# Kernel optimization log

Measured on AMD Instinct MI355X. Metric: run time of the kernel, lower is better.

Reference implementation:

```python
import jax, jax.numpy as jnp
import numpy as np

B, N, K = 16, 4096, 128

def setup_inputs() -> dict:
    key = jax.random.key(0)
    k1, k2, k3, k4, k5 = jax.random.split(key, 5)
    positions = jax.random.normal(k1, (B, N, 3), dtype=jnp.float32) * 5.0
    neighbors = jax.random.randint(k2, (B, N, K), 0, N, dtype=jnp.int32)
    neighbor_mask = (jax.random.uniform(k3, (B, N, K)) < 0.9).astype(jnp.float32)
    cell = jax.random.normal(k4, (B, 3, 3), dtype=jnp.float32) + 10.0 * jnp.eye(3, dtype=jnp.float32)
    cell_offsets = jax.random.randint(k5, (B, N, K, 3), -1, 2).astype(jnp.float32)
    return {
        "positions": positions,
        "neighbors": neighbors,
        "neighbor_mask": neighbor_mask,
        "cell": cell,
        "cell_offsets": cell_offsets,
    }

def reference(positions, neighbors, neighbor_mask, cell, cell_offsets):
    # Gather neighbor positions: [B,N,K,3]
    pos_j = jax.vmap(lambda p, n: p[n])(positions, neighbors)
    # Relative vectors r_j - r_i
    dist_vec = pos_j - positions[:, :, None, :]
    # Periodic boundary correction: offsets @ cell, [B,N,K,3]
    dist_vec = dist_vec + jnp.einsum("bnkd,bde->bnke", cell_offsets, cell)
    sq = jnp.sum(dist_vec * dist_vec, axis=-1)  # [B,N,K]
    mask = neighbor_mask > 0
    # Masked distances (safe sqrt: avoid sqrt(0) grad issues on masked entries)
    distances = jnp.where(mask, jnp.sqrt(jnp.where(mask, sq, 1.0)), 0.0)
    return distances
```

## Files before the change

kernel.cpp:

```cpp
#include <hip/hip_runtime.h>
#include <math.h>

constexpr int B = 16;
constexpr int N = 4096;
constexpr int K = 128;

constexpr int ROWS_PER_BLOCK = 128;
constexpr int THREADS = 1024;
constexpr int CHUNKS  = 4;


struct Chunk {
    int4   jj;
    float4 mm, o0, o1, o2;
};

__device__ __forceinline__ void load_chunk(Chunk& c,
                                           const int*   __restrict__ nbr,
                                           const float* __restrict__ mask,
                                           const float* __restrict__ offs,
                                           size_t e0) {
    c.jj = *(const int4*)  (nbr  + e0);
    c.mm = *(const float4*)(mask + e0);
    c.o0 = *(const float4*)(offs + e0 * 3);
    c.o1 = *(const float4*)(offs + e0 * 3 + 4);
    c.o2 = *(const float4*)(offs + e0 * 3 + 8);
}

__global__ __launch_bounds__(THREADS, 8)
void pairwise_dist_pipe(const float* __restrict__ pos,
                        const int*   __restrict__ nbr,
                        const float* __restrict__ mask,
                        const float* __restrict__ cell,
                        const float* __restrict__ offs,
                        float*       __restrict__ out) {
    __shared__ float4 spos[N];

    const int tid   = threadIdx.x;
    const int b     = blockIdx.x >> 5;
    const int rblk  = blockIdx.x & 31;
    const int nbase = rblk * ROWS_PER_BLOCK;

    {
        const float4* __restrict__ pb4 =
            (const float4*)(pos + (size_t)b * N * 3);
        const float4 r0 = pb4[tid * 3 + 0];
        const float4 r1 = pb4[tid * 3 + 1];
        const float4 r2 = pb4[tid * 3 + 2];
        const int a0 = tid * 4;
        spos[a0 + 0] = make_float4(r0.x, r0.y, r0.z, 0.f);
        spos[a0 + 1] = make_float4(r0.w, r1.x, r1.y, 0.f);
        spos[a0 + 2] = make_float4(r1.z, r1.w, r2.x, 0.f);
        spos[a0 + 3] = make_float4(r2.y, r2.z, r2.w, 0.f);
    }

    const float* __restrict__ cb = cell + b * 9;
    const float c00 = cb[0], c01 = cb[1], c02 = cb[2];
    const float c10 = cb[3], c11 = cb[4], c12 = cb[5];
    const float c20 = cb[6], c21 = cb[7], c22 = cb[8];

    __syncthreads();

    const size_t blockElemBase = ((size_t)b * N + nbase) * K;

    Chunk cur;
    load_chunk(cur, nbr, mask, offs, blockElemBase + (size_t)tid * 4);

#pragma unroll
    for (int c = 0; c < CHUNKS; ++c) {
        Chunk nxt;
        if (c + 1 < CHUNKS) {
            const size_t eN = blockElemBase + (size_t)(c + 1) * 4096 +
                              (size_t)tid * 4;
            load_chunk(nxt, nbr, mask, offs, eN);
        }

        const int    eLocal = c * 4096 + tid * 4;
        const size_t e0     = blockElemBase + eLocal;
        const int    n      = nbase + (eLocal >> 7);
        const float4 pi     = spos[n];

        const float ox[4] = {cur.o0.x, cur.o0.w, cur.o1.z, cur.o2.y};
        const float oy[4] = {cur.o0.y, cur.o1.x, cur.o1.w, cur.o2.z};
        const float oz[4] = {cur.o0.z, cur.o1.y, cur.o2.x, cur.o2.w};
        const int   j [4] = {cur.jj.x, cur.jj.y, cur.jj.z, cur.jj.w};
        const float m [4] = {cur.mm.x, cur.mm.y, cur.mm.z, cur.mm.w};

        float res[4];
#pragma unroll
        for (int i = 0; i < 4; ++i) {
            const float4 pj = spos[j[i]];
            const float dx = (pj.x - pi.x) + ox[i] * c00 + oy[i] * c10 + oz[i] * c20;
            const float dy = (pj.y - pi.y) + ox[i] * c01 + oy[i] * c11 + oz[i] * c21;
            const float dz = (pj.z - pi.z) + ox[i] * c02 + oy[i] * c12 + oz[i] * c22;
            const float sq = dx * dx + dy * dy + dz * dz;
            res[i] = (m[i] > 0.0f) ? sqrtf(sq) : 0.0f;
        }

        *(float4*)(out + e0) = make_float4(res[0], res[1], res[2], res[3]);

        cur = nxt;
    }
}

extern "C" void kernel_launch(void* const* d_in, const int* in_sizes, int n_in,
                              void* d_out, int out_size, void* d_ws, size_t ws_size,
                              hipStream_t stream) {
    const float* positions     = (const float*)d_in[0];
    const int*   neighbors     = (const int*)  d_in[1];
    const float* neighbor_mask = (const float*)d_in[2];
    const float* cell          = (const float*)d_in[3];
    const float* cell_offsets  = (const float*)d_in[4];
    float*       out           = (float*)d_out;

    const int blocks = B * (N / ROWS_PER_BLOCK);

    pairwise_dist_pipe<<<blocks, THREADS, 0, stream>>>(
        positions, neighbors, neighbor_mask, cell, cell_offsets, out);
}
```

Before: 215.5 us.

## Deepen load pipeline to a 4-chunk window with nontemporal loads and stores

Each block now covers 256 rows in 8 chunks and keeps four chunks of neighbor, mask and offset loads in flight, instead of prefetching one chunk ahead. Streaming loads and the output store use nontemporal builtins so they do not pollute cache. The shared-memory position staging is amortized over twice as many rows, which halves the number of blocks. The costs are more registers per thread (occupancy hint lowered from 8 to 4) and only 256 blocks left to fill the GPU.

```diff
diff --git a/kernel.cpp b/kernel.cpp
--- a/kernel.cpp
+++ b/kernel.cpp
@@ -5,14 +5,18 @@
 constexpr int N = 4096;
 constexpr int K = 128;
 
-constexpr int ROWS_PER_BLOCK = 128;
+constexpr int ROWS_PER_BLOCK = 256;
 constexpr int THREADS = 1024;
-constexpr int CHUNKS  = 4;
+constexpr int CHUNKS  = 8;
+constexpr int WINDOW  = 4;
+
+typedef float fx4 __attribute__((ext_vector_type(4)));
+typedef int   ix4 __attribute__((ext_vector_type(4)));
 
 
 struct Chunk {
-    int4   jj;
-    float4 mm, o0, o1, o2;
+    ix4 jj;
+    fx4 mm, o0, o1, o2;
 };
 
 __device__ __forceinline__ void load_chunk(Chunk& c,
@@ -20,38 +24,37 @@
                                            const float* __restrict__ mask,
                                            const float* __restrict__ offs,
                                            size_t e0) {
-    c.jj = *(const int4*)  (nbr  + e0);
-    c.mm = *(const float4*)(mask + e0);
-    c.o0 = *(const float4*)(offs + e0 * 3);
-    c.o1 = *(const float4*)(offs + e0 * 3 + 4);
-    c.o2 = *(const float4*)(offs + e0 * 3 + 8);
+    c.jj = __builtin_nontemporal_load((const ix4*)(nbr  + e0));
+    c.mm = __builtin_nontemporal_load((const fx4*)(mask + e0));
+    c.o0 = __builtin_nontemporal_load((const fx4*)(offs + e0 * 3));
+    c.o1 = __builtin_nontemporal_load((const fx4*)(offs + e0 * 3 + 4));
+    c.o2 = __builtin_nontemporal_load((const fx4*)(offs + e0 * 3 + 8));
 }
 
-__global__ __launch_bounds__(THREADS, 8)
-void pairwise_dist_pipe(const float* __restrict__ pos,
-                        const int*   __restrict__ nbr,
-                        const float* __restrict__ mask,
-                        const float* __restrict__ cell,
-                        const float* __restrict__ offs,
-                        float*       __restrict__ out) {
-    __shared__ float4 spos[N];
+__global__ __launch_bounds__(THREADS, 4)
+void pairwise_dist_mlp(const float* __restrict__ pos,
+                       const int*   __restrict__ nbr,
+                       const float* __restrict__ mask,
+                       const float* __restrict__ cell,
+                       const float* __restrict__ offs,
+                       float*       __restrict__ out) {
+    __shared__ fx4 spos[N];
 
     const int tid   = threadIdx.x;
-    const int b     = blockIdx.x >> 5;
-    const int rblk  = blockIdx.x & 31;
+    const int b     = blockIdx.x >> 4;
+    const int rblk  = blockIdx.x & 15;
     const int nbase = rblk * ROWS_PER_BLOCK;
 
     {
-        const float4* __restrict__ pb4 =
-            (const float4*)(pos + (size_t)b * N * 3);
-        const float4 r0 = pb4[tid * 3 + 0];
-        const float4 r1 = pb4[tid * 3 + 1];
-        const float4 r2 = pb4[tid * 3 + 2];
+        const fx4* __restrict__ pb4 = (const fx4*)(pos + (size_t)b * N * 3);
+        const fx4 r0 = pb4[tid * 3 + 0];
+        const fx4 r1 = pb4[tid * 3 + 1];
+        const fx4 r2 = pb4[tid * 3 + 2];
         const int a0 = tid * 4;
-        spos[a0 + 0] = make_float4(r0.x, r0.y, r0.z, 0.f);
-        spos[a0 + 1] = make_float4(r0.w, r1.x, r1.y, 0.f);
-        spos[a0 + 2] = make_float4(r1.z, r1.w, r2.x, 0.f);
-        spos[a0 + 3] = make_float4(r2.y, r2.z, r2.w, 0.f);
+        spos[a0 + 0] = (fx4){r0.x, r0.y, r0.z, 0.f};
+        spos[a0 + 1] = (fx4){r0.w, r1.x, r1.y, 0.f};
+        spos[a0 + 2] = (fx4){r1.z, r1.w, r2.x, 0.f};
+        spos[a0 + 3] = (fx4){r2.y, r2.z, r2.w, 0.f};
     }
 
     const float* __restrict__ cb = cell + b * 9;
@@ -63,22 +66,25 @@
 
     const size_t blockElemBase = ((size_t)b * N + nbase) * K;
 
-    Chunk cur;
-    load_chunk(cur, nbr, mask, offs, blockElemBase + (size_t)tid * 4);
+    Chunk win[WINDOW];
+#pragma unroll
+    for (int c = 0; c < WINDOW; ++c)
+        load_chunk(win[c], nbr, mask, offs,
+                   blockElemBase + (size_t)c * 4096 + (size_t)tid * 4);
 
 #pragma unroll
     for (int c = 0; c < CHUNKS; ++c) {
-        Chunk nxt;
-        if (c + 1 < CHUNKS) {
-            const size_t eN = blockElemBase + (size_t)(c + 1) * 4096 +
-                              (size_t)tid * 4;
-            load_chunk(nxt, nbr, mask, offs, eN);
-        }
+        const Chunk cur = win[c % WINDOW];
 
         const int    eLocal = c * 4096 + tid * 4;
         const size_t e0     = blockElemBase + eLocal;
         const int    n      = nbase + (eLocal >> 7);
-        const float4 pi     = spos[n];
+        const fx4    pi     = spos[n];
+
+        if (c + WINDOW < CHUNKS)
+            load_chunk(win[c % WINDOW], nbr, mask, offs,
+                       blockElemBase + (size_t)(c + WINDOW) * 4096 +
+                       (size_t)tid * 4);
 
         const float ox[4] = {cur.o0.x, cur.o0.w, cur.o1.z, cur.o2.y};
         const float oy[4] = {cur.o0.y, cur.o1.x, cur.o1.w, cur.o2.z};
@@ -89,7 +95,7 @@
         float res[4];
 #pragma unroll
         for (int i = 0; i < 4; ++i) {
-            const float4 pj = spos[j[i]];
+            const fx4 pj = spos[j[i]];
             const float dx = (pj.x - pi.x) + ox[i] * c00 + oy[i] * c10 + oz[i] * c20;
             const float dy = (pj.y - pi.y) + ox[i] * c01 + oy[i] * c11 + oz[i] * c21;
             const float dz = (pj.z - pi.z) + ox[i] * c02 + oy[i] * c12 + oz[i] * c22;
@@ -97,9 +103,8 @@
             res[i] = (m[i] > 0.0f) ? sqrtf(sq) : 0.0f;
         }
 
-        *(float4*)(out + e0) = make_float4(res[0], res[1], res[2], res[3]);
-
-        cur = nxt;
+        const fx4 r = {res[0], res[1], res[2], res[3]};
+        __builtin_nontemporal_store(r, (fx4*)(out + e0));
     }
 }
 
@@ -115,6 +120,6 @@
 
     const int blocks = B * (N / ROWS_PER_BLOCK);
 
-    pairwise_dist_pipe<<<blocks, THREADS, 0, stream>>>(
+    pairwise_dist_mlp<<<blocks, THREADS, 0, stream>>>(
         positions, neighbors, neighbor_mask, cell, cell_offsets, out);
 }
```

Measured after the change: 204.1 us. 1.06x faster.
